# Optimization experiments

Hardware: AMD Instinct MI355X
Metric: run time of the kernel (lower is better)

The kernel has to match this reference:

```python
import jax, jax.numpy as jnp
import numpy as np

B, H, W, C = 8, 56, 56, 192
HEADS, K, PAD = 6, 3, 1
KK = K * K
HEAD_DIM = C // HEADS
SCALE = HEAD_DIM ** -0.5


def setup_inputs() -> dict:
    key = jax.random.key(0)
    ks = jax.random.split(key, 6)
    s = lambda fan_in: 1.0 / np.sqrt(fan_in)
    return {
        "x": jax.random.normal(ks[0], (B, H, W, C), jnp.float32),
        "Wv": jax.random.normal(ks[1], (C, C), jnp.float32) * s(C),
        "Wa": jax.random.normal(ks[2], (C, KK * KK * HEADS), jnp.float32) * s(C),
        "ba": jax.random.normal(ks[3], (KK * KK * HEADS,), jnp.float32) * s(C),
        "Wp": jax.random.normal(ks[4], (C, C), jnp.float32) * s(C),
        "bp": jax.random.normal(ks[5], (C,), jnp.float32) * s(C),
    }


def _unfold(v_nchw):
    # im2col, kernel 3, pad 1, stride 1 -> (B, C, 9, H, W); kernel pos row-major like nn.Unfold
    vp = jnp.pad(v_nchw, ((0, 0), (0, 0), (PAD, PAD), (PAD, PAD)))
    return jnp.stack([vp[:, :, i:i + H, j:j + W] for i in range(K) for j in range(K)], axis=2)


def _fold(cols):
    # col2im scatter-add: cols (B, C, 9, H, W) -> (B, C, H, W)
    out = jnp.zeros((cols.shape[0], cols.shape[1], H + 2 * PAD, W + 2 * PAD), cols.dtype)
    idx = 0
    for i in range(K):
        for j in range(K):
            out = out.at[:, :, i:i + H, j:j + W].add(cols[:, :, idx])
            idx += 1
    return out[:, :, PAD:PAD + H, PAD:PAD + W]


def reference(x, Wv, Wa, ba, Wp, bp):
    hw = H * W
    # values: linear then unfold into per-pixel kxk windows
    v = jnp.einsum("bhwc,cd->bhwd", x, Wv)              # (B,H,W,C)
    v = _unfold(v.transpose(0, 3, 1, 2))                 # (B,C,9,H,W)
    v = v.reshape(B, HEADS, HEAD_DIM, KK, hw)
    v = v.transpose(0, 1, 4, 3, 2)                       # (B,heads,HW,9,c)
    # dynamic attention weights (stride=1 -> pool is identity)
    a = jnp.einsum("bhwc,ck->bhwk", x, Wa) + ba          # (B,H,W,81*heads)
    a = a.reshape(B, hw, HEADS, KK, KK).transpose(0, 2, 1, 3, 4)
    a = jax.nn.softmax(a * SCALE, axis=-1)               # (B,heads,HW,9,9)
    o = jnp.einsum("bnpkl,bnplc->bnpkc", a, v)           # (B,heads,HW,9,c)
    o = o.transpose(0, 1, 4, 3, 2).reshape(B, C, KK, H, W)
    o = _fold(o)                                          # (B,C,H,W)
    o = o.transpose(0, 2, 3, 1)                           # NHWC
    return jnp.einsum("bhwc,cd->bhwd", o, Wp) + bp
```

## Files before the change

kernel.cpp:

```cpp
#include <hip/hip_runtime.h>
#include <hip/hip_bf16.h>

constexpr int NH = 56, NW = 56, NC = 192, AJ = 486;
constexpr int HWP = NH * NW;
constexpr int NPIX = 8 * HWP;
constexpr float SCALE = 0.17677669529663687f;

typedef __bf16 bf16x8 __attribute__((ext_vector_type(8)));
typedef float f32x4 __attribute__((ext_vector_type(4)));

__device__ __forceinline__ void gload16(const void* g, void* l) {
  __builtin_amdgcn_global_load_lds(
      (const __attribute__((address_space(1))) void*)g,
      (__attribute__((address_space(3))) void*)l, 16, 0, 0);
}

__global__ __launch_bounds__(256) void k_prep2(const float* __restrict__ x,
                                               const float* __restrict__ Wv,
                                               const float* __restrict__ Wa,
                                               const float* __restrict__ Wp,
                                               __bf16* __restrict__ xb,
                                               __bf16* __restrict__ Wvt,
                                               __bf16* __restrict__ Wat,
                                               __bf16* __restrict__ Wpt) {
  const int bid = blockIdx.x;
  if (bid < 144) {
    const int i = bid * 256 + threadIdx.x;
    const int n = i / 192, k = i - n * 192;
    Wvt[i] = (__bf16)Wv[k * 192 + n];
    Wpt[i] = (__bf16)Wp[k * 192 + n];
  } else if (bid < 528) {
    const int i = (bid - 144) * 256 + threadIdx.x;
    const int n = i / 192, k = i - n * 192;
    Wat[i] = (n < 486) ? (__bf16)Wa[k * 486 + n] : (__bf16)0.f;
  } else {
    const size_t i = (size_t)(bid - 528) * 256 + threadIdx.x;
    const float* src = x + i * 8;
    const float4 f0 = *(const float4*)src;
    const float4 f1 = *(const float4*)(src + 4);
    bf16x8 o8;
    o8[0] = (__bf16)f0.x; o8[1] = (__bf16)f0.y;
    o8[2] = (__bf16)f0.z; o8[3] = (__bf16)f0.w;
    o8[4] = (__bf16)f1.x; o8[5] = (__bf16)f1.y;
    o8[6] = (__bf16)f1.z; o8[7] = (__bf16)f1.w;
    *(bf16x8*)(xb + i * 8) = o8;
  }
}

template <int MODE>
__global__ __launch_bounds__(256) void k_gemm_nn(const __bf16* __restrict__ A,
                                                 const __bf16* __restrict__ Bt,
                                                 const float* __restrict__ bias,
                                                 void* __restrict__ C) {
  __shared__ __bf16 As[64 * 32];
  __shared__ __bf16 Bs[192 * 32];
  const int m0 = blockIdx.x * 64;
  const int t = threadIdx.x, lane = t & 63, w = t >> 6;
  const int wm = w >> 1, wn = w & 1;
  f32x4 acc[2][6];
  #pragma unroll
  for (int mi = 0; mi < 2; ++mi)
    #pragma unroll
    for (int nj = 0; nj < 6; ++nj) acc[mi][nj] = (f32x4){0.f, 0.f, 0.f, 0.f};

  const int cA = w * 64 + lane;
  const int rowA = cA >> 2, kcA = (cA & 3) * 8;

  for (int k0 = 0; k0 < 192; k0 += 32) {
    __syncthreads();
    gload16(A + (size_t)(m0 + rowA) * 192 + k0 + kcA, &As[(w * 64) * 8]);
    #pragma unroll
    for (int i = 0; i < 3; ++i) {
      const int cB = i * 256 + w * 64 + lane;
      const int rowB = cB >> 2, kcB = (cB & 3) * 8;
      gload16(Bt + (size_t)rowB * 192 + k0 + kcB, &Bs[(i * 256 + w * 64) * 8]);
    }
    __syncthreads();
    bf16x8 af[2], bfr[6];
    #pragma unroll
    for (int mi = 0; mi < 2; ++mi)
      af[mi] = *(const bf16x8*)&As[(wm * 32 + mi * 16 + (lane & 15)) * 32 + (lane >> 4) * 8];
    #pragma unroll
    for (int nj = 0; nj < 6; ++nj)
      bfr[nj] = *(const bf16x8*)&Bs[(wn * 96 + nj * 16 + (lane & 15)) * 32 + (lane >> 4) * 8];
    #pragma unroll
    for (int mi = 0; mi < 2; ++mi)
      #pragma unroll
      for (int nj = 0; nj < 6; ++nj)
        acc[mi][nj] = __builtin_amdgcn_mfma_f32_16x16x32_bf16(af[mi], bfr[nj], acc[mi][nj], 0, 0, 0);
  }
  const int col_l = lane & 15, rq4 = (lane >> 4) * 4;
  #pragma unroll
  for (int nj = 0; nj < 6; ++nj) {
    const int gn = wn * 96 + nj * 16 + col_l;
    const float bv = (MODE == 2) ? bias[gn] : 0.f;
    #pragma unroll
    for (int mi = 0; mi < 2; ++mi) {
      const int gm = m0 + wm * 32 + mi * 16 + rq4;
      #pragma unroll
      for (int r = 0; r < 4; ++r) {
        if (MODE == 0)
          ((__bf16*)C)[(size_t)(gm + r) * 192 + gn] = (__bf16)acc[mi][nj][r];
        else
          ((float*)C)[(size_t)(gm + r) * 192 + gn] = acc[mi][nj][r] + bv;
      }
    }
  }
}

__global__ __launch_bounds__(256) void k_gemmT2(const __bf16* __restrict__ Wat,
                                                const __bf16* __restrict__ xb,
                                                const float* __restrict__ ba,
                                                __bf16* __restrict__ lgT) {
  __shared__ __bf16 As[128 * 32];
  __shared__ __bf16 Bs[128 * 32];
  const int m0 = blockIdx.x * 128, n0 = blockIdx.y * 128;
  const int t = threadIdx.x, lane = t & 63, w = t >> 6;
  const int wm = w >> 1, wn = w & 1;
  f32x4 acc[4][4];
  #pragma unroll
  for (int mi = 0; mi < 4; ++mi)
    #pragma unroll
    for (int nj = 0; nj < 4; ++nj) acc[mi][nj] = (f32x4){0.f, 0.f, 0.f, 0.f};

  for (int k0 = 0; k0 < 192; k0 += 32) {
    __syncthreads();
    #pragma unroll
    for (int i = 0; i < 2; ++i) {
      const int c = i * 256 + w * 64 + lane;
      const int row = c >> 2, kc = (c & 3) * 8;
      gload16(Wat + (size_t)(m0 + row) * 192 + k0 + kc, &As[(i * 256 + w * 64) * 8]);
      gload16(xb + (size_t)(n0 + row) * 192 + k0 + kc, &Bs[(i * 256 + w * 64) * 8]);
    }
    __syncthreads();
    bf16x8 af[4], bfr[4];
    #pragma unroll
    for (int mi = 0; mi < 4; ++mi)
      af[mi] = *(const bf16x8*)&As[(wm * 64 + mi * 16 + (lane & 15)) * 32 + (lane >> 4) * 8];
    #pragma unroll
    for (int nj = 0; nj < 4; ++nj)
      bfr[nj] = *(const bf16x8*)&Bs[(wn * 64 + nj * 16 + (lane & 15)) * 32 + (lane >> 4) * 8];
    #pragma unroll
    for (int mi = 0; mi < 4; ++mi)
      #pragma unroll
      for (int nj = 0; nj < 4; ++nj)
        acc[mi][nj] = __builtin_amdgcn_mfma_f32_16x16x32_bf16(af[mi], bfr[nj], acc[mi][nj], 0, 0, 0);
  }
  const int col_l = lane & 15, rq4 = (lane >> 4) * 4;
  #pragma unroll
  for (int nj = 0; nj < 4; ++nj) {
    const int gn = n0 + wn * 64 + nj * 16 + col_l;
    #pragma unroll
    for (int mi = 0; mi < 4; ++mi) {
      const int gmb = m0 + wm * 64 + mi * 16 + rq4;
      #pragma unroll
      for (int r = 0; r < 4; ++r) {
        const int gm = gmb + r;
        if (gm < 486)
          lgT[(size_t)gm * NPIX + gn] = (__bf16)((acc[mi][nj][r] + ba[gm]) * SCALE);
      }
    }
  }
}

__global__ __launch_bounds__(256) void k_coef(const __bf16* __restrict__ lgT,
                                              __bf16* __restrict__ wcT) {
  const int p = blockIdx.x * 256 + threadIdx.x;
  const int head = blockIdx.y;
  const int b = p / HWP;
  const int yx = p - b * HWP;
  const int y = yx / NW, x = yx - y * NW;

  float wc[25];
  #pragma unroll
  for (int c = 0; c < 25; ++c) wc[c] = 0.f;

  #pragma unroll
  for (int ki = 0; ki < 3; ++ki) {
    const int h = y - ki + 1;
    if ((unsigned)h >= (unsigned)NH) continue;
    #pragma unroll
    for (int kj = 0; kj < 3; ++kj) {
      const int ww = x - kj + 1;
      if ((unsigned)ww >= (unsigned)NW) continue;
      const int src = b * HWP + h * NW + ww;
      const size_t base = (size_t)((head * 9 + ki * 3 + kj) * 9) * NPIX + src;
      float lt[9];
      #pragma unroll
      for (int l = 0; l < 9; ++l) lt[l] = (float)lgT[base + (size_t)l * NPIX];
      float m = lt[0];
      #pragma unroll
      for (int l = 1; l < 9; ++l) m = fmaxf(m, lt[l]);
      float s = 0.f;
      #pragma unroll
      for (int l = 0; l < 9; ++l) { lt[l] = __expf(lt[l] - m); s += lt[l]; }
      const float inv = 1.f / s;
      #pragma unroll
      for (int l = 0; l < 9; ++l) {
        const int li = l / 3, lj = l - li * 3;
        wc[(li - ki + 2) * 5 + (lj - kj + 2)] += lt[l] * inv;
      }
    }
  }
  #pragma unroll
  for (int c = 0; c < 25; ++c)
    wcT[(size_t)(head * 25 + c) * NPIX + p] = (__bf16)wc[c];
}

__global__ __launch_bounds__(192) void k_att2(const __bf16* __restrict__ v,
                                              const __bf16* __restrict__ wcT,
                                              __bf16* __restrict__ o) {
  const int p0 = blockIdx.x * 8;
  const int bb = p0 / HWP;
  const int yx0 = p0 - bb * HWP;
  const int y = yx0 / NW, x0 = yx0 - y * NW;
  const int t = threadIdx.x;

  __shared__ __bf16 vs[60][192];
  __shared__ float wcs[8][6][28];

  for (int i = t; i < 1440; i += 192) {
    const int cell = i / 24, ck = i - cell * 24;
    const int di = cell / 12, col = cell - di * 12;
    const int yy = y + di - 2, xx = x0 + col - 2;
    bf16x8 val;
    #pragma unroll
    for (int j = 0; j < 8; ++j) val[j] = (__bf16)0.f;
    if ((unsigned)yy < (unsigned)NH && (unsigned)xx < (unsigned)NW)
      val = *(const bf16x8*)&v[(size_t)(bb * HWP + yy * NW + xx) * 192 + ck * 8];
    *(bf16x8*)&vs[cell][ck * 8] = val;
  }
  if (t < 150) {
    const int head = t / 25, cc = t - head * 25;
    const bf16x8 w8 = *(const bf16x8*)&wcT[(size_t)t * NPIX + p0];
    #pragma unroll
    for (int q = 0; q < 8; ++q) wcs[q][head][cc] = (float)w8[q];
  }
  __syncthreads();

  const int ch = t, head = ch >> 5;
  float vr[5][12];
  #pragma unroll
  for (int di = 0; di < 5; ++di)
    #pragma unroll
    for (int col = 0; col < 12; ++col) vr[di][col] = (float)vs[di * 12 + col][ch];
  #pragma unroll
  for (int q = 0; q < 8; ++q) {
    float coef[25];
    #pragma unroll
    for (int i = 0; i < 6; ++i)
      *(float4*)&coef[i * 4] = *(const float4*)&wcs[q][head][i * 4];
    coef[24] = wcs[q][head][24];
    float s = 0.f;
    #pragma unroll
    for (int di = 0; di < 5; ++di)
      #pragma unroll
      for (int dj = 0; dj < 5; ++dj) s += coef[di * 5 + dj] * vr[di][q + dj];
    o[(size_t)(p0 + q) * 192 + ch] = (__bf16)s;
  }
}

extern "C" void kernel_launch(void* const* d_in, const int* in_sizes, int n_in,
                              void* d_out, int out_size, void* d_ws,
                              size_t ws_size, hipStream_t stream) {
  (void)in_sizes; (void)n_in; (void)out_size; (void)ws_size;
  const float* x  = (const float*)d_in[0];
  const float* Wv = (const float*)d_in[1];
  const float* Wa = (const float*)d_in[2];
  const float* ba = (const float*)d_in[3];
  const float* Wp = (const float*)d_in[4];
  const float* bp = (const float*)d_in[5];

  char* ws = (char*)d_ws;
  __bf16* Wvt = (__bf16*)(ws);
  __bf16* Wat = (__bf16*)(ws + 73728);
  __bf16* Wpt = (__bf16*)(ws + 270336);
  __bf16* xb  = (__bf16*)(ws + 344064);
  __bf16* v_ws = (__bf16*)(ws + 9977856);
  __bf16* lgT = (__bf16*)(ws + 19611648);
  __bf16* wcT = (__bf16*)(ws + 43997184);
  __bf16* o_ws = (__bf16*)(ws + 19611648);

  k_prep2<<<2880, 256, 0, stream>>>(x, Wv, Wa, Wp, xb, Wvt, Wat, Wpt);
  k_gemm_nn<0><<<392, 256, 0, stream>>>(xb, Wvt, nullptr, v_ws);
  k_gemmT2<<<dim3(4, 196), 256, 0, stream>>>(Wat, xb, ba, lgT);
  k_coef<<<dim3(98, 6), 256, 0, stream>>>(lgT, wcT);
  k_att2<<<NPIX / 8, 192, 0, stream>>>(v_ws, wcT, o_ws);
  k_gemm_nn<2><<<392, 256, 0, stream>>>(o_ws, Wpt, bp, (float*)d_out);
}
```

Measured before the change: 149.7 us.

## Merge value and logit GEMMs into one launch and retile output GEMM

The value projection GEMM and the attention-logit GEMM now run in a single kernel, with blockIdx.y choosing which GEMM each block computes. This removes one launch and lets the two GEMMs fill the GPU together. Both GEMMs now use 128-row tiles, the value GEMM taking 64-column N tiles. The output projection GEMM moves from 64x192 tiles on 392 blocks to 128x64 tiles on a 196x3 grid, giving more blocks. The cost is more branching inside the merged kernel, and a 64-wide N tile re-reads the A operand for each of the three N blocks.

```diff
diff --git a/kernel.cpp b/kernel.cpp
--- a/kernel.cpp
+++ b/kernel.cpp
@@ -47,118 +47,155 @@
   }
 }
 
-template <int MODE>
-__global__ __launch_bounds__(256) void k_gemm_nn(const __bf16* __restrict__ A,
-                                                 const __bf16* __restrict__ Bt,
-                                                 const float* __restrict__ bias,
-                                                 void* __restrict__ C) {
-  __shared__ __bf16 As[64 * 32];
-  __shared__ __bf16 Bs[192 * 32];
-  const int m0 = blockIdx.x * 64;
+__global__ __launch_bounds__(256) void k_mm(const __bf16* __restrict__ xb,
+                                            const __bf16* __restrict__ Wvt,
+                                            const __bf16* __restrict__ Wat,
+                                            const float* __restrict__ ba,
+                                            __bf16* __restrict__ v,
+                                            __bf16* __restrict__ lgT) {
+  __shared__ __bf16 As[128 * 32];
+  __shared__ __bf16 Bs[128 * 32];
   const int t = threadIdx.x, lane = t & 63, w = t >> 6;
   const int wm = w >> 1, wn = w & 1;
-  f32x4 acc[2][6];
-  #pragma unroll
-  for (int mi = 0; mi < 2; ++mi)
-    #pragma unroll
-    for (int nj = 0; nj < 6; ++nj) acc[mi][nj] = (f32x4){0.f, 0.f, 0.f, 0.f};
-
-  const int cA = w * 64 + lane;
-  const int rowA = cA >> 2, kcA = (cA & 3) * 8;
+  const bool vmode = (blockIdx.y < 3);
+  const __bf16* Aptr = vmode ? xb + (size_t)(blockIdx.x * 128) * 192
+                             : Wat + (size_t)((blockIdx.y - 3) * 128) * 192;
+  const __bf16* Bptr = vmode ? Wvt + (size_t)(blockIdx.y * 64) * 192
+                             : xb + (size_t)(blockIdx.x * 128) * 192;
+
+  f32x4 acc[4][4];
+  #pragma unroll
+  for (int mi = 0; mi < 4; ++mi)
+    #pragma unroll
+    for (int nj = 0; nj < 4; ++nj) acc[mi][nj] = (f32x4){0.f, 0.f, 0.f, 0.f};
 
   for (int k0 = 0; k0 < 192; k0 += 32) {
     __syncthreads();
-    gload16(A + (size_t)(m0 + rowA) * 192 + k0 + kcA, &As[(w * 64) * 8]);
-    #pragma unroll
-    for (int i = 0; i < 3; ++i) {
-      const int cB = i * 256 + w * 64 + lane;
-      const int rowB = cB >> 2, kcB = (cB & 3) * 8;
-      gload16(Bt + (size_t)rowB * 192 + k0 + kcB, &Bs[(i * 256 + w * 64) * 8]);
+    #pragma unroll
+    for (int i = 0; i < 2; ++i) {
+      const int c = i * 256 + w * 64 + lane;
+      gload16(Aptr + (size_t)(c >> 2) * 192 + k0 + (c & 3) * 8,
+              &As[(i * 256 + w * 64) * 8]);
+    }
+    {
+      const int c = w * 64 + lane;
+      gload16(Bptr + (size_t)(c >> 2) * 192 + k0 + (c & 3) * 8,
+              &Bs[(w * 64) * 8]);
+    }
+    if (!vmode) {
+      const int c = 256 + w * 64 + lane;
+      gload16(Bptr + (size_t)(c >> 2) * 192 + k0 + (c & 3) * 8,
+              &Bs[(256 + w * 64) * 8]);
     }
     __syncthreads();
-    bf16x8 af[2], bfr[6];
-    #pragma unroll
-    for (int mi = 0; mi < 2; ++mi)
-      af[mi] = *(const bf16x8*)&As[(wm * 32 + mi * 16 + (lane & 15)) * 32 + (lane >> 4) * 8];
-    #pragma unroll
-    for (int nj = 0; nj < 6; ++nj)
-      bfr[nj] = *(const bf16x8*)&Bs[(wn * 96 + nj * 16 + (lane & 15)) * 32 + (lane >> 4) * 8];
-    #pragma unroll
-    for (int mi = 0; mi < 2; ++mi)
-      #pragma unroll
-      for (int nj = 0; nj < 6; ++nj)
-        acc[mi][nj] = __builtin_amdgcn_mfma_f32_16x16x32_bf16(af[mi], bfr[nj], acc[mi][nj], 0, 0, 0);
+    bf16x8 af[4], bfr[4];
+    #pragma unroll
+    for (int mi = 0; mi < 4; ++mi)
+      af[mi] = *(const bf16x8*)&As[(wm * 64 + mi * 16 + (lane & 15)) * 32 + (lane >> 4) * 8];
+    if (vmode) {
+      #pragma unroll
+      for (int nj = 0; nj < 2; ++nj)
+        bfr[nj] = *(const bf16x8*)&Bs[(wn * 32 + nj * 16 + (lane & 15)) * 32 + (lane >> 4) * 8];
+      #pragma unroll
+      for (int mi = 0; mi < 4; ++mi)
+        #pragma unroll
+        for (int nj = 0; nj < 2; ++nj)
+          acc[mi][nj] = __builtin_amdgcn_mfma_f32_16x16x32_bf16(af[mi], bfr[nj], acc[mi][nj], 0, 0, 0);
+    } else {
+      #pragma unroll
+      for (int nj = 0; nj < 4; ++nj)
+        bfr[nj] = *(const bf16x8*)&Bs[(wn * 64 + nj * 16 + (lane & 15)) * 32 + (lane >> 4) * 8];
+      #pragma unroll
+      for (int mi = 0; mi < 4; ++mi)
+        #pragma unroll
+        for (int nj = 0; nj < 4; ++nj)
+          acc[mi][nj] = __builtin_amdgcn_mfma_f32_16x16x32_bf16(af[mi], bfr[nj], acc[mi][nj], 0, 0, 0);
+    }
   }
   const int col_l = lane & 15, rq4 = (lane >> 4) * 4;
-  #pragma unroll
-  for (int nj = 0; nj < 6; ++nj) {
-    const int gn = wn * 96 + nj * 16 + col_l;
-    const float bv = (MODE == 2) ? bias[gn] : 0.f;
-    #pragma unroll
-    for (int mi = 0; mi < 2; ++mi) {
-      const int gm = m0 + wm * 32 + mi * 16 + rq4;
-      #pragma unroll
-      for (int r = 0; r < 4; ++r) {
-        if (MODE == 0)
-          ((__bf16*)C)[(size_t)(gm + r) * 192 + gn] = (__bf16)acc[mi][nj][r];
-        else
-          ((float*)C)[(size_t)(gm + r) * 192 + gn] = acc[mi][nj][r] + bv;
+  if (vmode) {
+    #pragma unroll
+    for (int nj = 0; nj < 2; ++nj) {
+      const int gn = blockIdx.y * 64 + wn * 32 + nj * 16 + col_l;
+      #pragma unroll
+      for (int mi = 0; mi < 4; ++mi) {
+        const int gm = blockIdx.x * 128 + wm * 64 + mi * 16 + rq4;
+        #pragma unroll
+        for (int r = 0; r < 4; ++r)
+          v[(size_t)(gm + r) * 192 + gn] = (__bf16)acc[mi][nj][r];
       }
     }
-  }
-}
-
-__global__ __launch_bounds__(256) void k_gemmT2(const __bf16* __restrict__ Wat,
-                                                const __bf16* __restrict__ xb,
-                                                const float* __restrict__ ba,
-                                                __bf16* __restrict__ lgT) {
+  } else {
+    #pragma unroll
+    for (int nj = 0; nj < 4; ++nj) {
+      const int gn = blockIdx.x * 128 + wn * 64 + nj * 16 + col_l;
+      #pragma unroll
+      for (int mi = 0; mi < 4; ++mi) {
+        const int gmb = (blockIdx.y - 3) * 128 + wm * 64 + mi * 16 + rq4;
+        #pragma unroll
+        for (int r = 0; r < 4; ++r) {
+          const int gm = gmb + r;
+          if (gm < 486)
+            lgT[(size_t)gm * NPIX + gn] = (__bf16)((acc[mi][nj][r] + ba[gm]) * SCALE);
+        }
+      }
+    }
+  }
+}
+
+__global__ __launch_bounds__(256) void k_gemm_out(const __bf16* __restrict__ A,
+                                                  const __bf16* __restrict__ Bt,
+                                                  const float* __restrict__ bias,
+                                                  float* __restrict__ C) {
   __shared__ __bf16 As[128 * 32];
-  __shared__ __bf16 Bs[128 * 32];
-  const int m0 = blockIdx.x * 128, n0 = blockIdx.y * 128;
+  __shared__ __bf16 Bs[64 * 32];
+  const int m0 = blockIdx.x * 128, n0 = blockIdx.y * 64;
   const int t = threadIdx.x, lane = t & 63, w = t >> 6;
   const int wm = w >> 1, wn = w & 1;
-  f32x4 acc[4][4];
+  f32x4 acc[4][2];
   #pragma unroll
   for (int mi = 0; mi < 4; ++mi)
     #pragma unroll
-    for (int nj = 0; nj < 4; ++nj) acc[mi][nj] = (f32x4){0.f, 0.f, 0.f, 0.f};
+    for (int nj = 0; nj < 2; ++nj) acc[mi][nj] = (f32x4){0.f, 0.f, 0.f, 0.f};
 
   for (int k0 = 0; k0 < 192; k0 += 32) {
     __syncthreads();
     #pragma unroll
     for (int i = 0; i < 2; ++i) {
       const int c = i * 256 + w * 64 + lane;
-      const int row = c >> 2, kc = (c & 3) * 8;
-      gload16(Wat + (size_t)(m0 + row) * 192 + k0 + kc, &As[(i * 256 + w * 64) * 8]);
-      gload16(xb + (size_t)(n0 + row) * 192 + k0 + kc, &Bs[(i * 256 + w * 64) * 8]);
+      gload16(A + (size_t)(m0 + (c >> 2)) * 192 + k0 + (c & 3) * 8,
+              &As[(i * 256 + w * 64) * 8]);
+    }
+    {
+      const int c = w * 64 + lane;
+      gload16(Bt + (size_t)(n0 + (c >> 2)) * 192 + k0 + (c & 3) * 8,
+              &Bs[(w * 64) * 8]);
     }
     __syncthreads();
-    bf16x8 af[4], bfr[4];
+    bf16x8 af[4], bfr[2];
     #pragma unroll
     for (int mi = 0; mi < 4; ++mi)
       af[mi] = *(const bf16x8*)&As[(wm * 64 + mi * 16 + (lane & 15)) * 32 + (lane >> 4) * 8];
     #pragma unroll
-    for (int nj = 0; nj < 4; ++nj)
-      bfr[nj] = *(const bf16x8*)&Bs[(wn * 64 + nj * 16 + (lane & 15)) * 32 + (lane >> 4) * 8];
+    for (int nj = 0; nj < 2; ++nj)
+      bfr[nj] = *(const bf16x8*)&Bs[(wn * 32 + nj * 16 + (lane & 15)) * 32 + (lane >> 4) * 8];
     #pragma unroll
     for (int mi = 0; mi < 4; ++mi)
       #pragma unroll
-      for (int nj = 0; nj < 4; ++nj)
+      for (int nj = 0; nj < 2; ++nj)
         acc[mi][nj] = __builtin_amdgcn_mfma_f32_16x16x32_bf16(af[mi], bfr[nj], acc[mi][nj], 0, 0, 0);
   }
   const int col_l = lane & 15, rq4 = (lane >> 4) * 4;
   #pragma unroll
-  for (int nj = 0; nj < 4; ++nj) {
-    const int gn = n0 + wn * 64 + nj * 16 + col_l;
+  for (int nj = 0; nj < 2; ++nj) {
+    const int gn = n0 + wn * 32 + nj * 16 + col_l;
+    const float bv = bias[gn];
     #pragma unroll
     for (int mi = 0; mi < 4; ++mi) {
-      const int gmb = m0 + wm * 64 + mi * 16 + rq4;
-      #pragma unroll
-      for (int r = 0; r < 4; ++r) {
-        const int gm = gmb + r;
-        if (gm < 486)
-          lgT[(size_t)gm * NPIX + gn] = (__bf16)((acc[mi][nj][r] + ba[gm]) * SCALE);
-      }
+      const int gm = m0 + wm * 64 + mi * 16 + rq4;
+      #pragma unroll
+      for (int r = 0; r < 4; ++r)
+        C[(size_t)(gm + r) * 192 + gn] = acc[mi][nj][r] + bv;
     }
   }
 }
@@ -282,9 +319,8 @@
   __bf16* o_ws = (__bf16*)(ws + 19611648);
 
   k_prep2<<<2880, 256, 0, stream>>>(x, Wv, Wa, Wp, xb, Wvt, Wat, Wpt);
-  k_gemm_nn<0><<<392, 256, 0, stream>>>(xb, Wvt, nullptr, v_ws);
-  k_gemmT2<<<dim3(4, 196), 256, 0, stream>>>(Wat, xb, ba, lgT);
+  k_mm<<<dim3(196, 7), 256, 0, stream>>>(xb, Wvt, Wat, ba, v_ws, lgT);
   k_coef<<<dim3(98, 6), 256, 0, stream>>>(lgT, wcT);
   k_att2<<<NPIX / 8, 192, 0, stream>>>(v_ws, wcT, o_ws);
-  k_gemm_nn<2><<<392, 256, 0, stream>>>(o_ws, Wpt, bp, (float*)d_out);
-}
+  k_gemm_out<<<dim3(196, 3), 256, 0, stream>>>(o_ws, Wpt, bp, (float*)d_out);
+}
```

After: 156.6 us. +4.6%, slower.

## Pre-tile GEMM operands into 64x192 blocks and use single-shot full-K tiles

Applied to the files above, without the earlier changes.

Operands (x, weights, attention output) are written into a tiled 64-row by 32-k blocked layout so each GEMM block can load its entire 64x192 A and B tiles with contiguous 16-byte global-to-LDS copies in one pass. All three GEMMs share one kernel with a 64x64 output tile and no K-loop synchronisation. This removes per-k-step barriers and strided loads, at the cost of larger LDS use per block (48KB), more blocks that reload the shared operand, and a scattered write in the attention kernel.

```diff
diff --git a/kernel.cpp b/kernel.cpp
--- a/kernel.cpp
+++ b/kernel.cpp
@@ -5,6 +5,7 @@
 constexpr int HWP = NH * NW;
 constexpr int NPIX = 8 * HWP;
 constexpr float SCALE = 0.17677669529663687f;
+constexpr int TS = 12288;
 
 typedef __bf16 bf16x8 __attribute__((ext_vector_type(8)));
 typedef float f32x4 __attribute__((ext_vector_type(4)));
@@ -15,7 +16,11 @@
       (__attribute__((address_space(3))) void*)l, 16, 0, 0);
 }
 
-__global__ __launch_bounds__(256) void k_prep2(const float* __restrict__ x,
+__device__ __forceinline__ size_t toff(int row, int k) {
+  return (size_t)(row >> 6) * TS + (k >> 5) * 2048 + (row & 63) * 32 + (k & 31);
+}
+
+__global__ __launch_bounds__(256) void k_prep3(const float* __restrict__ x,
                                                const float* __restrict__ Wv,
                                                const float* __restrict__ Wa,
                                                const float* __restrict__ Wp,
@@ -27,15 +32,17 @@
   if (bid < 144) {
     const int i = bid * 256 + threadIdx.x;
     const int n = i / 192, k = i - n * 192;
-    Wvt[i] = (__bf16)Wv[k * 192 + n];
-    Wpt[i] = (__bf16)Wp[k * 192 + n];
+    const size_t d = toff(n, k);
+    Wvt[d] = (__bf16)Wv[k * 192 + n];
+    Wpt[d] = (__bf16)Wp[k * 192 + n];
   } else if (bid < 528) {
     const int i = (bid - 144) * 256 + threadIdx.x;
     const int n = i / 192, k = i - n * 192;
-    Wat[i] = (n < 486) ? (__bf16)Wa[k * 486 + n] : (__bf16)0.f;
+    Wat[toff(n, k)] = (n < 486) ? (__bf16)Wa[k * 486 + n] : (__bf16)0.f;
   } else {
     const size_t i = (size_t)(bid - 528) * 256 + threadIdx.x;
-    const float* src = x + i * 8;
+    const int pix = (int)(i / 24), c8 = (int)(i % 24) * 8;
+    const float* src = x + (size_t)pix * 192 + c8;
     const float4 f0 = *(const float4*)src;
     const float4 f1 = *(const float4*)(src + 4);
     bf16x8 o8;
@@ -43,121 +50,71 @@
     o8[2] = (__bf16)f0.z; o8[3] = (__bf16)f0.w;
     o8[4] = (__bf16)f1.x; o8[5] = (__bf16)f1.y;
     o8[6] = (__bf16)f1.z; o8[7] = (__bf16)f1.w;
-    *(bf16x8*)(xb + i * 8) = o8;
+    *(bf16x8*)(xb + toff(pix, c8)) = o8;
   }
 }
 
 template <int MODE>
-__global__ __launch_bounds__(256) void k_gemm_nn(const __bf16* __restrict__ A,
-                                                 const __bf16* __restrict__ Bt,
-                                                 const float* __restrict__ bias,
-                                                 void* __restrict__ C) {
-  __shared__ __bf16 As[64 * 32];
-  __shared__ __bf16 Bs[192 * 32];
-  const int m0 = blockIdx.x * 64;
+__global__ __launch_bounds__(256) void k_gemm1(const __bf16* __restrict__ At,
+                                               const __bf16* __restrict__ Bt,
+                                               const float* __restrict__ bias,
+                                               void* __restrict__ C) {
+  __shared__ __bf16 As[64 * 192];
+  __shared__ __bf16 Bs[64 * 192];
   const int t = threadIdx.x, lane = t & 63, w = t >> 6;
   const int wm = w >> 1, wn = w & 1;
-  f32x4 acc[2][6];
+  const int a_tile = (MODE == 1) ? blockIdx.y : blockIdx.x;
+  const int b_tile = (MODE == 1) ? blockIdx.x : blockIdx.y;
+  const __bf16* Asrc = At + (size_t)a_tile * TS;
+  const __bf16* Bsrc = Bt + (size_t)b_tile * TS;
+  #pragma unroll
+  for (int i = 0; i < 6; ++i) {
+    const int cb = i * 256 + w * 64;
+    gload16(Asrc + (size_t)(cb + lane) * 8, &As[cb * 8]);
+    gload16(Bsrc + (size_t)(cb + lane) * 8, &Bs[cb * 8]);
+  }
+  f32x4 acc[2][2];
   #pragma unroll
   for (int mi = 0; mi < 2; ++mi)
     #pragma unroll
-    for (int nj = 0; nj < 6; ++nj) acc[mi][nj] = (f32x4){0.f, 0.f, 0.f, 0.f};
-
-  const int cA = w * 64 + lane;
-  const int rowA = cA >> 2, kcA = (cA & 3) * 8;
-
-  for (int k0 = 0; k0 < 192; k0 += 32) {
-    __syncthreads();
-    gload16(A + (size_t)(m0 + rowA) * 192 + k0 + kcA, &As[(w * 64) * 8]);
-    #pragma unroll
-    for (int i = 0; i < 3; ++i) {
-      const int cB = i * 256 + w * 64 + lane;
-      const int rowB = cB >> 2, kcB = (cB & 3) * 8;
-      gload16(Bt + (size_t)rowB * 192 + k0 + kcB, &Bs[(i * 256 + w * 64) * 8]);
-    }
-    __syncthreads();
-    bf16x8 af[2], bfr[6];
+    for (int nj = 0; nj < 2; ++nj) acc[mi][nj] = (f32x4){0.f, 0.f, 0.f, 0.f};
+  __syncthreads();
+  #pragma unroll
+  for (int ks = 0; ks < 6; ++ks) {
+    bf16x8 af[2], bfr[2];
     #pragma unroll
     for (int mi = 0; mi < 2; ++mi)
-      af[mi] = *(const bf16x8*)&As[(wm * 32 + mi * 16 + (lane & 15)) * 32 + (lane >> 4) * 8];
-    #pragma unroll
-    for (int nj = 0; nj < 6; ++nj)
-      bfr[nj] = *(const bf16x8*)&Bs[(wn * 96 + nj * 16 + (lane & 15)) * 32 + (lane >> 4) * 8];
+      af[mi] = *(const bf16x8*)&As[(ks * 64 + wm * 32 + mi * 16 + (lane & 15)) * 32 + (lane >> 4) * 8];
+    #pragma unroll
+    for (int nj = 0; nj < 2; ++nj)
+      bfr[nj] = *(const bf16x8*)&Bs[(ks * 64 + wn * 32 + nj * 16 + (lane & 15)) * 32 + (lane >> 4) * 8];
     #pragma unroll
     for (int mi = 0; mi < 2; ++mi)
       #pragma unroll
-      for (int nj = 0; nj < 6; ++nj)
+      for (int nj = 0; nj < 2; ++nj)
         acc[mi][nj] = __builtin_amdgcn_mfma_f32_16x16x32_bf16(af[mi], bfr[nj], acc[mi][nj], 0, 0, 0);
   }
   const int col_l = lane & 15, rq4 = (lane >> 4) * 4;
   #pragma unroll
-  for (int nj = 0; nj < 6; ++nj) {
-    const int gn = wn * 96 + nj * 16 + col_l;
-    const float bv = (MODE == 2) ? bias[gn] : 0.f;
+  for (int nj = 0; nj < 2; ++nj) {
+    const int ln = wn * 32 + nj * 16 + col_l;
     #pragma unroll
     for (int mi = 0; mi < 2; ++mi) {
-      const int gm = m0 + wm * 32 + mi * 16 + rq4;
+      const int lm = wm * 32 + mi * 16 + rq4;
       #pragma unroll
       for (int r = 0; r < 4; ++r) {
-        if (MODE == 0)
-          ((__bf16*)C)[(size_t)(gm + r) * 192 + gn] = (__bf16)acc[mi][nj][r];
-        else
-          ((float*)C)[(size_t)(gm + r) * 192 + gn] = acc[mi][nj][r] + bv;
-      }
-    }
-  }
-}
-
-__global__ __launch_bounds__(256) void k_gemmT2(const __bf16* __restrict__ Wat,
-                                                const __bf16* __restrict__ xb,
-                                                const float* __restrict__ ba,
-                                                __bf16* __restrict__ lgT) {
-  __shared__ __bf16 As[128 * 32];
-  __shared__ __bf16 Bs[128 * 32];
-  const int m0 = blockIdx.x * 128, n0 = blockIdx.y * 128;
-  const int t = threadIdx.x, lane = t & 63, w = t >> 6;
-  const int wm = w >> 1, wn = w & 1;
-  f32x4 acc[4][4];
-  #pragma unroll
-  for (int mi = 0; mi < 4; ++mi)
-    #pragma unroll
-    for (int nj = 0; nj < 4; ++nj) acc[mi][nj] = (f32x4){0.f, 0.f, 0.f, 0.f};
-
-  for (int k0 = 0; k0 < 192; k0 += 32) {
-    __syncthreads();
-    #pragma unroll
-    for (int i = 0; i < 2; ++i) {
-      const int c = i * 256 + w * 64 + lane;
-      const int row = c >> 2, kc = (c & 3) * 8;
-      gload16(Wat + (size_t)(m0 + row) * 192 + k0 + kc, &As[(i * 256 + w * 64) * 8]);
-      gload16(xb + (size_t)(n0 + row) * 192 + k0 + kc, &Bs[(i * 256 + w * 64) * 8]);
-    }
-    __syncthreads();
-    bf16x8 af[4], bfr[4];
-    #pragma unroll
-    for (int mi = 0; mi < 4; ++mi)
-      af[mi] = *(const bf16x8*)&As[(wm * 64 + mi * 16 + (lane & 15)) * 32 + (lane >> 4) * 8];
-    #pragma unroll
-    for (int nj = 0; nj < 4; ++nj)
-      bfr[nj] = *(const bf16x8*)&Bs[(wn * 64 + nj * 16 + (lane & 15)) * 32 + (lane >> 4) * 8];
-    #pragma unroll
-    for (int mi = 0; mi < 4; ++mi)
-      #pragma unroll
-      for (int nj = 0; nj < 4; ++nj)
-        acc[mi][nj] = __builtin_amdgcn_mfma_f32_16x16x32_bf16(af[mi], bfr[nj], acc[mi][nj], 0, 0, 0);
-  }
-  const int col_l = lane & 15, rq4 = (lane >> 4) * 4;
-  #pragma unroll
-  for (int nj = 0; nj < 4; ++nj) {
-    const int gn = n0 + wn * 64 + nj * 16 + col_l;
-    #pragma unroll
-    for (int mi = 0; mi < 4; ++mi) {
-      const int gmb = m0 + wm * 64 + mi * 16 + rq4;
-      #pragma unroll
-      for (int r = 0; r < 4; ++r) {
-        const int gm = gmb + r;
-        if (gm < 486)
-          lgT[(size_t)gm * NPIX + gn] = (__bf16)((acc[mi][nj][r] + ba[gm]) * SCALE);
+        const float val = acc[mi][nj][r];
+        if (MODE == 0) {
+          const int pix = blockIdx.x * 64 + lm + r, ch = blockIdx.y * 64 + ln;
+          ((__bf16*)C)[(size_t)pix * 192 + ch] = (__bf16)val;
+        } else if (MODE == 1) {
+          const int j = blockIdx.y * 64 + lm + r, pix = blockIdx.x * 64 + ln;
+          if (j < 486)
+            ((__bf16*)C)[(size_t)j * NPIX + pix] = (__bf16)((val + bias[j]) * SCALE);
+        } else {
+          const int pix = blockIdx.x * 64 + lm + r, ch = blockIdx.y * 64 + ln;
+          ((float*)C)[(size_t)pix * 192 + ch] = val + bias[ch];
+        }
       }
     }
   }
@@ -244,6 +201,7 @@
   for (int di = 0; di < 5; ++di)
     #pragma unroll
     for (int col = 0; col < 12; ++col) vr[di][col] = (float)vs[di * 12 + col][ch];
+  const size_t obase = (size_t)(p0 >> 6) * TS + (ch >> 5) * 2048 + (p0 & 63) * 32 + (ch & 31);
   #pragma unroll
   for (int q = 0; q < 8; ++q) {
     float coef[25];
@@ -256,7 +214,7 @@
     for (int di = 0; di < 5; ++di)
       #pragma unroll
       for (int dj = 0; dj < 5; ++dj) s += coef[di * 5 + dj] * vr[di][q + dj];
-    o[(size_t)(p0 + q) * 192 + ch] = (__bf16)s;
+    o[obase + q * 32] = (__bf16)s;
   }
 }
 
@@ -281,10 +239,10 @@
   __bf16* wcT = (__bf16*)(ws + 43997184);
   __bf16* o_ws = (__bf16*)(ws + 19611648);
 
-  k_prep2<<<2880, 256, 0, stream>>>(x, Wv, Wa, Wp, xb, Wvt, Wat, Wpt);
-  k_gemm_nn<0><<<392, 256, 0, stream>>>(xb, Wvt, nullptr, v_ws);
-  k_gemmT2<<<dim3(4, 196), 256, 0, stream>>>(Wat, xb, ba, lgT);
+  k_prep3<<<2880, 256, 0, stream>>>(x, Wv, Wa, Wp, xb, Wvt, Wat, Wpt);
+  k_gemm1<0><<<dim3(392, 3), 256, 0, stream>>>(xb, Wvt, nullptr, v_ws);
+  k_gemm1<1><<<dim3(392, 8), 256, 0, stream>>>(Wat, xb, ba, lgT);
   k_coef<<<dim3(98, 6), 256, 0, stream>>>(lgT, wcT);
   k_att2<<<NPIX / 8, 192, 0, stream>>>(v_ws, wcT, o_ws);
-  k_gemm_nn<2><<<392, 256, 0, stream>>>(o_ws, Wpt, bp, (float*)d_out);
-}
+  k_gemm1<2><<<dim3(392, 3), 256, 0, stream>>>(o_ws, Wpt, bp, (float*)d_out);
+}
```

After: 146.4 us. 2.2% less time.
